# Optimization experiments

Hardware: AMD Instinct MI355X
Metric: run time of the kernel (lower is better)

The kernel has to match this reference:

```python
import jax, jax.numpy as jnp
import numpy as np

DIM = 64
HEADS = 8
K_RATIOS = [0.5, 0.67, 0.75, 0.8]
BN_EPS = 1e-5


def conv3d(x, w, b, groups=1, pad=0):
    out = jax.lax.conv_general_dilated(
        x, w, window_strides=(1, 1, 1), padding=[(pad, pad)] * 3,
        dimension_numbers=('NCDHW', 'OIDHW', 'NCDHW'),
        feature_group_count=groups)
    return out + b[None, :, None, None, None]


def bn_eval(x, gamma, beta):
    # BatchNorm3d in inference mode with init running stats (mean=0, var=1)
    s = gamma / np.float32(np.sqrt(1.0 + BN_EPS))
    return x * s[None, :, None, None, None] + beta[None, :, None, None, None]


def setup_inputs() -> dict:
    key = jax.random.key(0)
    ks = jax.random.split(key, 12)
    def p(k, shape, scale=0.05):
        return jax.random.normal(k, shape, dtype=jnp.float32) * scale
    B, D, H, W = 2, 16, 64, 64
    return {
        'x': jax.random.normal(ks[0], (B, DIM, D, H, W), dtype=jnp.float32),
        'w_qkv': p(ks[1], (3 * DIM, DIM, 1, 1, 1)),
        'b_qkv': p(ks[2], (3 * DIM,)),
        'w_dw': p(ks[3], (3 * DIM, 1, 3, 3, 3)),
        'b_dw': p(ks[4], (3 * DIM,)),
        'temperature': jnp.ones((HEADS, 1, 1), jnp.float32),
        'attn_weights': jnp.ones((len(K_RATIOS),), jnp.float32),
        'w_recal': p(ks[5], (DIM, DIM, 1, 1, 1)),
        'b_recal': p(ks[6], (DIM,)),
        'bn1_g': jnp.ones((DIM,), jnp.float32),
        'bn1_b': jnp.zeros((DIM,), jnp.float32),
        'w_fus': p(ks[7], (DIM, 2 * DIM, 1, 1, 1)),
        'b_fus': p(ks[8], (DIM,)),
        'bn2_g': jnp.ones((DIM,), jnp.float32),
        'bn2_b': jnp.zeros((DIM,), jnp.float32),
        'w_proj': p(ks[9], (DIM, DIM, 1, 1, 1)),
        'b_proj': p(ks[10], (DIM,)),
    }


def reference(x, w_qkv, b_qkv, w_dw, b_dw, temperature, attn_weights,
              w_recal, b_recal, bn1_g, bn1_b, w_fus, b_fus, bn2_g, bn2_b,
              w_proj, b_proj):
    b, c, d, h, w = x.shape
    residual = x
    qkv = conv3d(conv3d(x, w_qkv, b_qkv), w_dw, b_dw, groups=3 * DIM, pad=1)
    q, k, v = jnp.split(qkv, 3, axis=1)
    def to_heads(t):  # b (head ch) d h w -> b head ch (d h w)
        return t.reshape(b, HEADS, c // HEADS, d * h * w)
    q, k, v = to_heads(q), to_heads(k), to_heads(v)
    # L2-normalize along token dim (torch F.normalize, eps=1e-12)
    q = q / jnp.maximum(jnp.linalg.norm(q, axis=-1, keepdims=True), 1e-12)
    k = k / jnp.maximum(jnp.linalg.norm(k, axis=-1, keepdims=True), 1e-12)
    C = q.shape[2]
    attn = jnp.einsum('bhin,bhjn->bhij', q, k) * temperature[None]  # (b,head,C,C)
    soft_w = jax.nn.softmax(attn_weights)
    weighted = 0.0
    for i, ratio in enumerate(K_RATIOS):
        kv = int(C * ratio)
        idx = jax.lax.top_k(attn, kv)[1]                      # (b,head,C,kv)
        mask = jax.nn.one_hot(idx, C, dtype=attn.dtype).sum(-2) > 0
        probs = jax.nn.softmax(jnp.where(mask, attn, -jnp.inf), axis=-1)
        out = jnp.einsum('bhij,bhjn->bhin', probs, v)          # (b,head,C,N)
        weighted = weighted + soft_w[i] * out.reshape(b, c, d, h, w)
    recalib = jax.nn.sigmoid(bn_eval(conv3d(weighted, w_recal, b_recal), bn1_g, bn1_b))
    enhanced = weighted * recalib
    fused = jnp.concatenate([enhanced, residual], axis=1)
    output = bn_eval(conv3d(fused, w_fus, b_fus), bn2_g, bn2_b)
    output = conv3d(output, w_proj, b_proj)
    return output
```

## Files before the change

### kernel.cpp

```cpp
#include <hip/hip_runtime.h>
#include <math.h>

#define NPOS 65536
#define DD 16
#define HHH 64
#define WWW 64
#define K3CHUNK 64

typedef __attribute__((ext_vector_type(8))) short bf16x8;
typedef __attribute__((ext_vector_type(4))) short s16x4;
typedef __attribute__((ext_vector_type(4))) float f32x4;
typedef __attribute__((ext_vector_type(2))) _Float16 f16x2;

static __device__ __forceinline__ short f2bf(float f) {
    union { float f; unsigned u; } v; v.f = f;
    unsigned r = (v.u + 0x7FFFu + ((v.u >> 16) & 1u)) >> 16;
    return (short)r;
}
static __device__ __forceinline__ float bf2f(short s) {
    union { unsigned u; float f; } v; v.u = ((unsigned)(unsigned short)s) << 16;
    return v.f;
}
static __device__ __forceinline__ f16x2 i2h(int i) {
    union { int i; f16x2 h; } v; v.i = i; return v.h;
}
static __device__ __forceinline__ int h2i(f16x2 h) {
    union { int i; f16x2 h; } v; v.h = h; return v.i;
}
static __device__ __forceinline__ float fdot2f(f16x2 a, f16x2 b, float c) {
#if __has_builtin(__builtin_amdgcn_fdot2)
    return __builtin_amdgcn_fdot2(a, b, c, false);
#else
    return fmaf((float)a[0], (float)b[0], fmaf((float)a[1], (float)b[1], c));
#endif
}

__global__ void k0_prep(const float* __restrict__ Wq,
                        const float* __restrict__ Wr, const float* __restrict__ Wf,
                        const float* __restrict__ Wp,
                        const float* __restrict__ brec,
                        const float* __restrict__ bn1g, const float* __restrict__ bn1b,
                        const float* __restrict__ bfus,
                        const float* __restrict__ bn2g, const float* __restrict__ bn2b,
                        short* __restrict__ WqA, short* __restrict__ WrA,
                        short* __restrict__ WfA, short* __restrict__ WpA,
                        float* __restrict__ bias1, float* __restrict__ bias2) {
    const float invs = 1.0f / sqrtf(1.0f + 1e-5f);
    int idx = blockIdx.x * 256 + threadIdx.x;
    if (idx < 12288) {
        int e = idx & 7, l = (idx >> 3) & 63, m = (idx >> 9) & 3;
        int t = (idx >> 11) & 1, c = idx >> 12;
        int out = c*64 + 16*m + (l & 15), k = 32*t + ((l >> 4) << 3) + e;
        WqA[idx] = f2bf(Wq[out*64 + k]);
        return;
    }
    int i = idx - 12288;
    if (i < 4096) {
        int e = i & 7, l = (i >> 3) & 63, m = (i >> 9) & 3, t = (i >> 11) & 1;
        int out = 16*m + (l & 15), k = 32*t + ((l >> 4) << 3) + e;
        WrA[i] = f2bf(Wr[out*64 + k] * bn1g[out] * invs);
        return;
    }
    i -= 4096;
    if (i < 8192) {
        int e = i & 7, l = (i >> 3) & 63, m = (i >> 9) & 3, t = (i >> 11) & 3;
        int out = 16*m + (l & 15), k = 32*t + ((l >> 4) << 3) + e;
        WfA[i] = f2bf(Wf[out*128 + k] * bn2g[out] * invs);
        return;
    }
    i -= 8192;
    if (i < 4096) {
        int e = i & 7, l = (i >> 3) & 63, m = (i >> 9) & 3, t = (i >> 11) & 1;
        int out = 16*m + (l & 15), k = 32*t + ((l >> 4) << 3) + e;
        WpA[i] = f2bf(Wp[out*64 + k]);
        return;
    }
    i -= 4096;
    if (i < 64)       bias1[i]    = brec[i]    * bn1g[i]    * invs + bn1b[i];
    else if (i < 128) bias2[i-64] = bfus[i-64] * bn2g[i-64] * invs + bn2b[i-64];
}

__global__ __launch_bounds__(256) void k1_qkv(const float* __restrict__ x,
        const short* __restrict__ WqA, const float* __restrict__ bq,
        short* __restrict__ qkv) {
    __shared__ __align__(16) float Xs[64 * 64];
    const int tid = threadIdx.x, lane = tid & 63, wv = tid >> 6;
    const int blk = blockIdx.x;
    const int b = blk >> 10, n0 = (blk & 1023) << 6;
    const float* xg = x + ((long long)b * 64) * NPOS + n0;
    #pragma unroll
    for (int kk = 0; kk < 4; ++kk) {
        int idx = tid + kk * 256;
        int ch = idx >> 4, p = (idx & 15) << 2;
        *(float4*)(Xs + ch * 64 + p) = *(const float4*)(xg + (long long)ch * NPOS + p);
    }
    const int bcol  = wv * 16 + (lane & 15);
    const int bk    = (lane >> 4) << 3;
    const int drow0 = (lane >> 4) << 2;
    __syncthreads();

    bf16x8 B0, B1;
    #pragma unroll
    for (int e = 0; e < 8; ++e) B0[e] = f2bf(Xs[(bk + e) * 64 + bcol]);
    #pragma unroll
    for (int e = 0; e < 8; ++e) B1[e] = f2bf(Xs[(32 + bk + e) * 64 + bcol]);

    short* outb = qkv + ((long long)b * 192) * NPOS + n0 + bcol;
    #pragma unroll
    for (int c = 0; c < 3; ++c) {
        #pragma unroll
        for (int m = 0; m < 4; ++m) {
            bf16x8 A0 = *(const bf16x8*)(WqA + (((c * 2 + 0) * 4 + m) * 64 + lane) * 8);
            bf16x8 A1 = *(const bf16x8*)(WqA + (((c * 2 + 1) * 4 + m) * 64 + lane) * 8);
            f32x4 a = {0.f, 0.f, 0.f, 0.f};
            a = __builtin_amdgcn_mfma_f32_16x16x32_bf16(A0, B0, a, 0, 0, 0);
            a = __builtin_amdgcn_mfma_f32_16x16x32_bf16(A1, B1, a, 0, 0, 0);
            float4 bb = *(const float4*)(bq + c * 64 + 16 * m + drow0);
            a[0] += bb.x; a[1] += bb.y; a[2] += bb.z; a[3] += bb.w;
            #pragma unroll
            for (int r = 0; r < 4; ++r)
                outb[(long long)(c * 64 + 16 * m + drow0 + r) * NPOS] = f2bf(a[r]);
        }
    }
}

__global__ __launch_bounds__(256) void k2_dw(const short* __restrict__ qkv,
        const float* __restrict__ Wd, const float* __restrict__ bd,
        short* __restrict__ qkv2) {
    __shared__ __align__(16) _Float16 tile[108 * 72];
    __shared__ unsigned wpk01[9], wpk2z[9];
    __shared__ float bsh[1];
    const int tid = threadIdx.x;
    const int lane = tid & 63;
    const int bc  = blockIdx.x >> 4;
    const int sub = blockIdx.x & 15;
    const int d0  = (sub >> 2) << 2;
    const int h0  = (sub & 3) << 4;
    const int c   = bc % 192;

    if (tid < 9) {
        const float* wb = Wd + c * 27 + tid * 3;
        f16x2 a = {(_Float16)wb[0], (_Float16)wb[1]};
        f16x2 z = {(_Float16)wb[2], (_Float16)0.f};
        wpk01[tid] = (unsigned)h2i(a);
        wpk2z[tid] = (unsigned)h2i(z);
    }
    if (tid == 31) bsh[0] = bd[c];

    const short* in = qkv + (long long)bc * NPOS;
    for (int i = tid; i < 864; i += 256) {
        const int r = i >> 3, q8 = i & 7;
        const int dd = r / 18;
        const int hh = r - dd * 18;
        const int d = d0 + dd - 1;
        const int h = h0 + hh - 1;
        union { f16x2 h[4]; int4 i4; } u;
        u.i4 = make_int4(0, 0, 0, 0);
        if (d >= 0 && d < DD && h >= 0 && h < HHH) {
            bf16x8 raw = *(const bf16x8*)(in + (d << 12) + (h << 6) + (q8 << 3));
            #pragma unroll
            for (int e = 0; e < 4; ++e) {
                f16x2 hp = {(_Float16)bf2f(raw[2 * e]), (_Float16)bf2f(raw[2 * e + 1])};
                u.h[e] = hp;
            }
        }
        *(int4*)(tile + r * 72 + (q8 << 3)) = u.i4;
    }
    __syncthreads();

    unsigned w01r[9], w2zr[9];
    #pragma unroll
    for (int s = 0; s < 9; ++s) { w01r[s] = wpk01[s]; w2zr[s] = wpk2z[s]; }
    const float bias = bsh[0];

    const int wl = tid & 15;
    const int oh = tid >> 4;
    const int w0 = wl << 2;

    float acc[4][4];
    #pragma unroll
    for (int od = 0; od < 4; ++od)
        #pragma unroll
        for (int j = 0; j < 4; ++j) acc[od][j] = bias;

    #pragma unroll
    for (int kh = 0; kh < 3; ++kh) {
        #pragma unroll
        for (int dp = 0; dp < 6; ++dp) {
            const int2 dd2 = *(const int2*)(tile + (dp * 18 + oh + kh) * 72 + w0);
            int Ldw = __shfl(dd2.y, (lane + 63) & 63, 64);
            int Rdw = __shfl(dd2.x, (lane + 1) & 63, 64);
            Ldw = (wl == 0)  ? 0 : Ldw;
            Rdw = (wl == 15) ? 0 : Rdw;
            int pr[5];
            pr[0] = __builtin_amdgcn_alignbit(dd2.x, Ldw, 16);
            pr[1] = dd2.x;
            pr[2] = __builtin_amdgcn_alignbit(dd2.y, dd2.x, 16);
            pr[3] = dd2.y;
            pr[4] = __builtin_amdgcn_alignbit(Rdw, dd2.y, 16);
            #pragma unroll
            for (int od = 0; od < 4; ++od) {
                const int kd = dp - od;
                if (kd < 0 || kd > 2) continue;
                const f16x2 w01 = i2h((int)w01r[kd * 3 + kh]);
                const f16x2 w2z = i2h((int)w2zr[kd * 3 + kh]);
                #pragma unroll
                for (int j = 0; j < 4; ++j) {
                    acc[od][j] = fdot2f(w01, i2h(pr[j]), acc[od][j]);
                    acc[od][j] = fdot2f(w2z, i2h(pr[j + 2]), acc[od][j]);
                }
            }
        }
    }
    short* outp = qkv2 + (long long)bc * NPOS + (h0 + oh) * 64 + w0;
    #pragma unroll
    for (int od = 0; od < 4; ++od) {
        s16x4 o;
        #pragma unroll
        for (int j = 0; j < 4; ++j) o[j] = f2bf(acc[od][j]);
        *(s16x4*)(outp + ((d0 + od) << 12)) = o;
    }
}

__global__ __launch_bounds__(256) void k3_gram(const short* __restrict__ qkv2,
                                               float* __restrict__ partial) {
    const int blk = blockIdx.x;
    const int chunk = blk & (K3CHUNK - 1);
    const int bh = blk >> 6;
    const int b = bh >> 3, h = bh & 7;
    const int tid = threadIdx.x, lane = tid & 63, wv = tid >> 6;
    const short* base = qkv2 + ((long long)b * 192 + h * 8) * NPOS;
    const int ch = lane & 15;
    const long long roff = (ch < 8 ? (long long)ch : (long long)(56 + ch)) * NPOS;
    const short* p = base + roff + chunk * 1024 + wv * 256 + ((lane >> 4) << 3);

    f32x4 a0 = {0.f, 0.f, 0.f, 0.f}, a1 = {0.f, 0.f, 0.f, 0.f};
    #pragma unroll
    for (int it = 0; it < 4; ++it) {
        bf16x8 f0 = *(const bf16x8*)(p + it * 64);
        bf16x8 f1 = *(const bf16x8*)(p + it * 64 + 32);
        a0 = __builtin_amdgcn_mfma_f32_16x16x32_bf16(f0, f0, a0, 0, 0, 0);
        a1 = __builtin_amdgcn_mfma_f32_16x16x32_bf16(f1, f1, a1, 0, 0, 0);
    }
    __shared__ float gs[4][256];
    #pragma unroll
    for (int r = 0; r < 4; ++r)
        gs[wv][(((lane >> 4) << 2) + r) * 16 + (lane & 15)] = a0[r] + a1[r];
    __syncthreads();
    const int row = tid >> 4, col = tid & 15;
    float v = gs[0][tid] + gs[1][tid] + gs[2][tid] + gs[3][tid];
    float* pp = partial + ((long long)bh * K3CHUNK + chunk) * 80;
    if (row < 8 && col >= 8)      pp[row * 8 + (col - 8)] = v;
    else if (row == col && row < 8) pp[64 + row] = v;
    else if (row == col)            pp[72 + row - 8] = v;
}

__global__ void k3b_reduce(const float* __restrict__ partial, float* __restrict__ gram) {
    int s = blockIdx.x * 256 + threadIdx.x;
    if (s >= 16 * 80) return;
    int bh = s / 80, slot = s % 80;
    float acc = 0.f;
    for (int c = 0; c < K3CHUNK; ++c)
        acc += partial[((long long)bh * K3CHUNK + c) * 80 + slot];
    gram[s] = acc;
}

__global__ void k4_combine(const float* __restrict__ gram, const float* __restrict__ temp,
                           const float* __restrict__ aw, float* __restrict__ P) {
    int t = threadIdx.x;
    if (t >= 128) return;
    int bh = t >> 3, i = t & 7;
    int h = bh & 7;
    const float* g = gram + bh * 80;
    float qn = fmaxf(sqrtf(g[64 + i]), 1e-12f);
    float tp = temp[h];
    float attn[8];
    #pragma unroll
    for (int j = 0; j < 8; ++j) {
        float kn = fmaxf(sqrtf(g[72 + j]), 1e-12f);
        attn[j] = g[i * 8 + j] / (qn * kn) * tp;
    }
    float awv[4];
    float am = -3.4e38f;
    for (int r = 0; r < 4; ++r) { awv[r] = aw[r]; am = fmaxf(am, awv[r]); }
    float asum = 0.f;
    for (int r = 0; r < 4; ++r) { awv[r] = expf(awv[r] - am); asum += awv[r]; }
    const int kvs[4] = {4, 5, 6, 6};
    float Pacc[8];
    #pragma unroll
    for (int j = 0; j < 8; ++j) Pacc[j] = 0.f;
    for (int r = 0; r < 4; ++r) {
        float sw = awv[r] / asum;
        int kv = kvs[r];
        bool sel[8];
        #pragma unroll
        for (int j = 0; j < 8; ++j) sel[j] = false;
        for (int m = 0; m < kv; ++m) {
            int best = 0; float bv = -3.4e38f;
            for (int j = 0; j < 8; ++j)
                if (!sel[j] && attn[j] > bv) { bv = attn[j]; best = j; }
            sel[best] = true;
        }
        float mx = -3.4e38f;
        for (int j = 0; j < 8; ++j) if (sel[j]) mx = fmaxf(mx, attn[j]);
        float es = 0.f, e[8];
        for (int j = 0; j < 8; ++j) { e[j] = sel[j] ? expf(attn[j] - mx) : 0.f; es += e[j]; }
        for (int j = 0; j < 8; ++j) Pacc[j] += sw * e[j] / es;
    }
    for (int j = 0; j < 8; ++j) P[t * 8 + j] = Pacc[j];
}

__global__ void k4b_pfrag(const float* __restrict__ P, short* __restrict__ PA) {
    int idx = blockIdx.x * 256 + threadIdx.x;
    int e = idx & 7, l = (idx >> 3) & 63, m = (idx >> 9) & 3;
    int t = (idx >> 11) & 1, b = idx >> 12;
    int out = 16*m + (l & 15), k = 32*t + ((l >> 4) << 3) + e;
    float v = ((k >> 3) == (out >> 3)) ? P[(b * 64 + out) * 8 + (k & 7)] : 0.f;
    PA[idx] = f2bf(v);
}

__global__ __launch_bounds__(256) void k5_tail(
        const short* __restrict__ qkv2, const float* __restrict__ x,
        const short* __restrict__ PA, const short* __restrict__ WrA,
        const short* __restrict__ WfA, const short* __restrict__ WpA,
        const float* __restrict__ bias1, const float* __restrict__ bias2,
        const float* __restrict__ bp, float* __restrict__ out) {
    __shared__ __align__(16) float As[64 * 64];
    __shared__ __align__(16) float Xs[64 * 64];
    const int tid = threadIdx.x, lane = tid & 63, wv = tid >> 6;
    const int blk = blockIdx.x;
    const int b = blk >> 10, n0 = (blk & 1023) << 6;
    const short* vg = qkv2 + ((long long)b * 192 + 128) * NPOS + n0;
    const float* xg = x + ((long long)b * 64) * NPOS + n0;
    #pragma unroll
    for (int kk = 0; kk < 4; ++kk) {
        int idx = tid + kk * 256;
        int ch = idx >> 4, p = (idx & 15) << 2;
        *(float4*)(Xs + ch * 64 + p) = *(const float4*)(xg + (long long)ch * NPOS + p);
    }
    #pragma unroll
    for (int kk = 0; kk < 2; ++kk) {
        int i = tid + kk * 256;
        int ch = i >> 3, p0 = (i & 7) << 3;
        bf16x8 raw = *(const bf16x8*)(vg + (long long)ch * NPOS + p0);
        *(float4*)(As + ch * 64 + p0) =
            make_float4(bf2f(raw[0]), bf2f(raw[1]), bf2f(raw[2]), bf2f(raw[3]));
        *(float4*)(As + ch * 64 + p0 + 4) =
            make_float4(bf2f(raw[4]), bf2f(raw[5]), bf2f(raw[6]), bf2f(raw[7]));
    }
    bf16x8 pA[2][4];
    #pragma unroll
    for (int t = 0; t < 2; ++t)
        #pragma unroll
        for (int m = 0; m < 4; ++m)
            pA[t][m] = *(const bf16x8*)(PA + (((b * 2 + t) * 4 + m) * 64 + lane) * 8);
    const int bcol  = wv * 16 + (lane & 15);
    const int bk    = (lane >> 4) << 3;
    const int drow0 = (lane >> 4) << 2;
    __syncthreads();

    auto loadB = [&](const float* S, int kbase) {
        bf16x8 r;
        #pragma unroll
        for (int e = 0; e < 8; ++e) r[e] = f2bf(S[(kbase + bk + e) * 64 + bcol]);
        return r;
    };

    f32x4 Dw[4];
    {
        bf16x8 B0 = loadB(As, 0), B1 = loadB(As, 32);
        #pragma unroll
        for (int m = 0; m < 4; ++m) {
            f32x4 a = {0.f, 0.f, 0.f, 0.f};
            a = __builtin_amdgcn_mfma_f32_16x16x32_bf16(pA[0][m], B0, a, 0, 0, 0);
            a = __builtin_amdgcn_mfma_f32_16x16x32_bf16(pA[1][m], B1, a, 0, 0, 0);
            Dw[m] = a;
        }
    }
    #pragma unroll
    for (int m = 0; m < 4; ++m)
        #pragma unroll
        for (int r = 0; r < 4; ++r)
            As[(16 * m + drow0 + r) * 64 + bcol] = Dw[m][r];

    float enh[4][4];
    {
        bf16x8 rA[2][4];
        #pragma unroll
        for (int t = 0; t < 2; ++t)
            #pragma unroll
            for (int m = 0; m < 4; ++m)
                rA[t][m] = *(const bf16x8*)(WrA + ((t * 4 + m) * 64 + lane) * 8);
        bf16x8 B0 = loadB(As, 0), B1 = loadB(As, 32);
        #pragma unroll
        for (int m = 0; m < 4; ++m) {
            f32x4 a = {0.f, 0.f, 0.f, 0.f};
            a = __builtin_amdgcn_mfma_f32_16x16x32_bf16(rA[0][m], B0, a, 0, 0, 0);
            a = __builtin_amdgcn_mfma_f32_16x16x32_bf16(rA[1][m], B1, a, 0, 0, 0);
            #pragma unroll
            for (int r = 0; r < 4; ++r) {
                float z = a[r] + bias1[16 * m + drow0 + r];
                enh[m][r] = Dw[m][r] / (1.f + expf(-z));
            }
        }
    }
    #pragma unroll
    for (int m = 0; m < 4; ++m)
        #pragma unroll
        for (int r = 0; r < 4; ++r)
            As[(16 * m + drow0 + r) * 64 + bcol] = enh[m][r];

    f32x4 D3[4];
    {
        bf16x8 fA[4][4];
        #pragma unroll
        for (int t = 0; t < 4; ++t)
            #pragma unroll
            for (int m = 0; m < 4; ++m)
                fA[t][m] = *(const bf16x8*)(WfA + ((t * 4 + m) * 64 + lane) * 8);
        bf16x8 B0 = loadB(As, 0), B1 = loadB(As, 32);
        bf16x8 B2 = loadB(Xs, 0), B3 = loadB(Xs, 32);
        #pragma unroll
        for (int m = 0; m < 4; ++m) {
            f32x4 a = {0.f, 0.f, 0.f, 0.f};
            a = __builtin_amdgcn_mfma_f32_16x16x32_bf16(fA[0][m], B0, a, 0, 0, 0);
            a = __builtin_amdgcn_mfma_f32_16x16x32_bf16(fA[1][m], B1, a, 0, 0, 0);
            a = __builtin_amdgcn_mfma_f32_16x16x32_bf16(fA[2][m], B2, a, 0, 0, 0);
            a = __builtin_amdgcn_mfma_f32_16x16x32_bf16(fA[3][m], B3, a, 0, 0, 0);
            #pragma unroll
            for (int r = 0; r < 4; ++r) a[r] += bias2[16 * m + drow0 + r];
            D3[m] = a;
        }
    }
    #pragma unroll
    for (int m = 0; m < 4; ++m)
        #pragma unroll
        for (int r = 0; r < 4; ++r)
            As[(16 * m + drow0 + r) * 64 + bcol] = D3[m][r];

    {
        bf16x8 qA[2][4];
        #pragma unroll
        for (int t = 0; t < 2; ++t)
            #pragma unroll
            for (int m = 0; m < 4; ++m)
                qA[t][m] = *(const bf16x8*)(WpA + ((t * 4 + m) * 64 + lane) * 8);
        bf16x8 B0 = loadB(As, 0), B1 = loadB(As, 32);
        float* outb = out + ((long long)b * 64) * NPOS + n0 + bcol;
        #pragma unroll
        for (int m = 0; m < 4; ++m) {
            f32x4 a = {0.f, 0.f, 0.f, 0.f};
            a = __builtin_amdgcn_mfma_f32_16x16x32_bf16(qA[0][m], B0, a, 0, 0, 0);
            a = __builtin_amdgcn_mfma_f32_16x16x32_bf16(qA[1][m], B1, a, 0, 0, 0);
            #pragma unroll
            for (int r = 0; r < 4; ++r)
                outb[(long long)(16 * m + drow0 + r) * NPOS] =
                    a[r] + bp[16 * m + drow0 + r];
        }
    }
}

extern "C" void kernel_launch(void* const* d_in, const int* in_sizes, int n_in,
                              void* d_out, int out_size, void* d_ws, size_t ws_size,
                              hipStream_t stream) {
    (void)in_sizes; (void)n_in; (void)out_size; (void)ws_size;
    const float* x     = (const float*)d_in[0];
    const float* w_qkv = (const float*)d_in[1];
    const float* b_qkv = (const float*)d_in[2];
    const float* w_dw  = (const float*)d_in[3];
    const float* b_dw  = (const float*)d_in[4];
    const float* temp  = (const float*)d_in[5];
    const float* aw    = (const float*)d_in[6];
    const float* w_rec = (const float*)d_in[7];
    const float* b_rec = (const float*)d_in[8];
    const float* bn1g  = (const float*)d_in[9];
    const float* bn1b  = (const float*)d_in[10];
    const float* w_fus = (const float*)d_in[11];
    const float* b_fus = (const float*)d_in[12];
    const float* bn2g  = (const float*)d_in[13];
    const float* bn2b  = (const float*)d_in[14];
    const float* w_prj = (const float*)d_in[15];
    const float* b_prj = (const float*)d_in[16];
    float* out = (float*)d_out;

    short* qkv  = (short*)d_ws;
    short* qkv2 = qkv + 25165824;
    float* part = (float*)(qkv2 + 25165824);
    float* gram = part + 163840;
    float* P    = gram + 1280;
    float* bias1 = P + 1024;
    float* bias2 = bias1 + 64;
    short* WqA  = (short*)(bias2 + 64);
    short* WrA  = WqA + 12288;
    short* WfA  = WrA + 4096;
    short* WpA  = WfA + 8192;
    short* PAb  = WpA + 4096;

    k0_prep<<<113, 256, 0, stream>>>(w_qkv, w_rec, w_fus, w_prj, b_rec, bn1g, bn1b,
                                     b_fus, bn2g, bn2b, WqA, WrA, WfA, WpA, bias1, bias2);
    k1_qkv<<<2048, 256, 0, stream>>>(x, WqA, b_qkv, qkv);
    k2_dw<<<6144, 256, 0, stream>>>(qkv, w_dw, b_dw, qkv2);
    k3_gram<<<16 * K3CHUNK, 256, 0, stream>>>(qkv2, part);
    k3b_reduce<<<5, 256, 0, stream>>>(part, gram);
    k4_combine<<<1, 128, 0, stream>>>(gram, temp, aw, P);
    k4b_pfrag<<<32, 256, 0, stream>>>(P, PAb);
    k5_tail<<<2048, 256, 0, stream>>>(qkv2, x, PAb, WrA, WfA, WpA,
                                      bias1, bias2, b_prj, out);
}
```

Measured before the change: 109.9 us.

## Switch intermediates to fp16 MFMA and fuse gram reduce, combine, pfrag kernels

Moves every intermediate buffer and MFMA from bf16 to fp16. This lets the depthwise conv tile load copy raw fp16 data straight into shared memory, where it previously converted bf16 to fp16 element by element. It also merges the three small kernels (gram reduction, top-k softmax combine, P fragment packing) into a single one-block kernel, removing two launches and their global round trips. The cost is fp16's narrower range on the activations, and the fused reduction now runs on only one block instead of five.

```diff
diff --git a/kernel.cpp b/kernel.cpp
--- a/kernel.cpp
+++ b/kernel.cpp
@@ -7,19 +7,16 @@
 #define WWW 64
 #define K3CHUNK 64
 
-typedef __attribute__((ext_vector_type(8))) short bf16x8;
+typedef __attribute__((ext_vector_type(8))) _Float16 h16x8;
 typedef __attribute__((ext_vector_type(4))) short s16x4;
 typedef __attribute__((ext_vector_type(4))) float f32x4;
 typedef __attribute__((ext_vector_type(2))) _Float16 f16x2;
 
-static __device__ __forceinline__ short f2bf(float f) {
-    union { float f; unsigned u; } v; v.f = f;
-    unsigned r = (v.u + 0x7FFFu + ((v.u >> 16) & 1u)) >> 16;
-    return (short)r;
-}
-static __device__ __forceinline__ float bf2f(short s) {
-    union { unsigned u; float f; } v; v.u = ((unsigned)(unsigned short)s) << 16;
-    return v.f;
+static __device__ __forceinline__ short f2h(float f) {
+    union { _Float16 h; short s; } v; v.h = (_Float16)f; return v.s;
+}
+static __device__ __forceinline__ float h2f(short s) {
+    union { short s; _Float16 h; } v; v.s = s; return (float)v.h;
 }
 static __device__ __forceinline__ f16x2 i2h(int i) {
     union { int i; f16x2 h; } v; v.i = i; return v.h;
@@ -51,28 +48,28 @@
         int e = idx & 7, l = (idx >> 3) & 63, m = (idx >> 9) & 3;
         int t = (idx >> 11) & 1, c = idx >> 12;
         int out = c*64 + 16*m + (l & 15), k = 32*t + ((l >> 4) << 3) + e;
-        WqA[idx] = f2bf(Wq[out*64 + k]);
+        WqA[idx] = f2h(Wq[out*64 + k]);
         return;
     }
     int i = idx - 12288;
     if (i < 4096) {
         int e = i & 7, l = (i >> 3) & 63, m = (i >> 9) & 3, t = (i >> 11) & 1;
         int out = 16*m + (l & 15), k = 32*t + ((l >> 4) << 3) + e;
-        WrA[i] = f2bf(Wr[out*64 + k] * bn1g[out] * invs);
+        WrA[i] = f2h(Wr[out*64 + k] * bn1g[out] * invs);
         return;
     }
     i -= 4096;
     if (i < 8192) {
         int e = i & 7, l = (i >> 3) & 63, m = (i >> 9) & 3, t = (i >> 11) & 3;
         int out = 16*m + (l & 15), k = 32*t + ((l >> 4) << 3) + e;
-        WfA[i] = f2bf(Wf[out*128 + k] * bn2g[out] * invs);
+        WfA[i] = f2h(Wf[out*128 + k] * bn2g[out] * invs);
         return;
     }
     i -= 8192;
     if (i < 4096) {
         int e = i & 7, l = (i >> 3) & 63, m = (i >> 9) & 3, t = (i >> 11) & 1;
         int out = 16*m + (l & 15), k = 32*t + ((l >> 4) << 3) + e;
-        WpA[i] = f2bf(Wp[out*64 + k]);
+        WpA[i] = f2h(Wp[out*64 + k]);
         return;
     }
     i -= 4096;
@@ -99,27 +96,27 @@
     const int drow0 = (lane >> 4) << 2;
     __syncthreads();
 
-    bf16x8 B0, B1;
-    #pragma unroll
-    for (int e = 0; e < 8; ++e) B0[e] = f2bf(Xs[(bk + e) * 64 + bcol]);
-    #pragma unroll
-    for (int e = 0; e < 8; ++e) B1[e] = f2bf(Xs[(32 + bk + e) * 64 + bcol]);
+    h16x8 B0, B1;
+    #pragma unroll
+    for (int e = 0; e < 8; ++e) B0[e] = (_Float16)Xs[(bk + e) * 64 + bcol];
+    #pragma unroll
+    for (int e = 0; e < 8; ++e) B1[e] = (_Float16)Xs[(32 + bk + e) * 64 + bcol];
 
     short* outb = qkv + ((long long)b * 192) * NPOS + n0 + bcol;
     #pragma unroll
     for (int c = 0; c < 3; ++c) {
         #pragma unroll
         for (int m = 0; m < 4; ++m) {
-            bf16x8 A0 = *(const bf16x8*)(WqA + (((c * 2 + 0) * 4 + m) * 64 + lane) * 8);
-            bf16x8 A1 = *(const bf16x8*)(WqA + (((c * 2 + 1) * 4 + m) * 64 + lane) * 8);
+            h16x8 A0 = *(const h16x8*)(WqA + (((c * 2 + 0) * 4 + m) * 64 + lane) * 8);
+            h16x8 A1 = *(const h16x8*)(WqA + (((c * 2 + 1) * 4 + m) * 64 + lane) * 8);
             f32x4 a = {0.f, 0.f, 0.f, 0.f};
-            a = __builtin_amdgcn_mfma_f32_16x16x32_bf16(A0, B0, a, 0, 0, 0);
-            a = __builtin_amdgcn_mfma_f32_16x16x32_bf16(A1, B1, a, 0, 0, 0);
+            a = __builtin_amdgcn_mfma_f32_16x16x32_f16(A0, B0, a, 0, 0, 0);
+            a = __builtin_amdgcn_mfma_f32_16x16x32_f16(A1, B1, a, 0, 0, 0);
             float4 bb = *(const float4*)(bq + c * 64 + 16 * m + drow0);
             a[0] += bb.x; a[1] += bb.y; a[2] += bb.z; a[3] += bb.w;
             #pragma unroll
             for (int r = 0; r < 4; ++r)
-                outb[(long long)(c * 64 + 16 * m + drow0 + r) * NPOS] = f2bf(a[r]);
+                outb[(long long)(c * 64 + 16 * m + drow0 + r) * NPOS] = f2h(a[r]);
         }
     }
 }
@@ -154,17 +151,10 @@
         const int hh = r - dd * 18;
         const int d = d0 + dd - 1;
         const int h = h0 + hh - 1;
-        union { f16x2 h[4]; int4 i4; } u;
-        u.i4 = make_int4(0, 0, 0, 0);
-        if (d >= 0 && d < DD && h >= 0 && h < HHH) {
-            bf16x8 raw = *(const bf16x8*)(in + (d << 12) + (h << 6) + (q8 << 3));
-            #pragma unroll
-            for (int e = 0; e < 4; ++e) {
-                f16x2 hp = {(_Float16)bf2f(raw[2 * e]), (_Float16)bf2f(raw[2 * e + 1])};
-                u.h[e] = hp;
-            }
-        }
-        *(int4*)(tile + r * 72 + (q8 << 3)) = u.i4;
+        int4 u = make_int4(0, 0, 0, 0);
+        if (d >= 0 && d < DD && h >= 0 && h < HHH)
+            u = *(const int4*)(in + (d << 12) + (h << 6) + (q8 << 3));
+        *(int4*)(tile + r * 72 + (q8 << 3)) = u;
     }
     __syncthreads();
 
@@ -217,7 +207,7 @@
     for (int od = 0; od < 4; ++od) {
         s16x4 o;
         #pragma unroll
-        for (int j = 0; j < 4; ++j) o[j] = f2bf(acc[od][j]);
+        for (int j = 0; j < 4; ++j) o[j] = f2h(acc[od][j]);
         *(s16x4*)(outp + ((d0 + od) << 12)) = o;
     }
 }
@@ -237,10 +227,10 @@
     f32x4 a0 = {0.f, 0.f, 0.f, 0.f}, a1 = {0.f, 0.f, 0.f, 0.f};
     #pragma unroll
     for (int it = 0; it < 4; ++it) {
-        bf16x8 f0 = *(const bf16x8*)(p + it * 64);
-        bf16x8 f1 = *(const bf16x8*)(p + it * 64 + 32);
-        a0 = __builtin_amdgcn_mfma_f32_16x16x32_bf16(f0, f0, a0, 0, 0, 0);
-        a1 = __builtin_amdgcn_mfma_f32_16x16x32_bf16(f1, f1, a1, 0, 0, 0);
+        h16x8 f0 = *(const h16x8*)(p + it * 64);
+        h16x8 f1 = *(const h16x8*)(p + it * 64 + 32);
+        a0 = __builtin_amdgcn_mfma_f32_16x16x32_f16(f0, f0, a0, 0, 0, 0);
+        a1 = __builtin_amdgcn_mfma_f32_16x16x32_f16(f1, f1, a1, 0, 0, 0);
     }
     __shared__ float gs[4][256];
     #pragma unroll
@@ -255,68 +245,69 @@
     else if (row == col)            pp[72 + row - 8] = v;
 }
 
-__global__ void k3b_reduce(const float* __restrict__ partial, float* __restrict__ gram) {
-    int s = blockIdx.x * 256 + threadIdx.x;
-    if (s >= 16 * 80) return;
-    int bh = s / 80, slot = s % 80;
-    float acc = 0.f;
-    for (int c = 0; c < K3CHUNK; ++c)
-        acc += partial[((long long)bh * K3CHUNK + c) * 80 + slot];
-    gram[s] = acc;
-}
-
-__global__ void k4_combine(const float* __restrict__ gram, const float* __restrict__ temp,
-                           const float* __restrict__ aw, float* __restrict__ P) {
-    int t = threadIdx.x;
-    if (t >= 128) return;
-    int bh = t >> 3, i = t & 7;
-    int h = bh & 7;
-    const float* g = gram + bh * 80;
-    float qn = fmaxf(sqrtf(g[64 + i]), 1e-12f);
-    float tp = temp[h];
-    float attn[8];
-    #pragma unroll
-    for (int j = 0; j < 8; ++j) {
-        float kn = fmaxf(sqrtf(g[72 + j]), 1e-12f);
-        attn[j] = g[i * 8 + j] / (qn * kn) * tp;
-    }
-    float awv[4];
-    float am = -3.4e38f;
-    for (int r = 0; r < 4; ++r) { awv[r] = aw[r]; am = fmaxf(am, awv[r]); }
-    float asum = 0.f;
-    for (int r = 0; r < 4; ++r) { awv[r] = expf(awv[r] - am); asum += awv[r]; }
-    const int kvs[4] = {4, 5, 6, 6};
-    float Pacc[8];
-    #pragma unroll
-    for (int j = 0; j < 8; ++j) Pacc[j] = 0.f;
-    for (int r = 0; r < 4; ++r) {
-        float sw = awv[r] / asum;
-        int kv = kvs[r];
-        bool sel[8];
-        #pragma unroll
-        for (int j = 0; j < 8; ++j) sel[j] = false;
-        for (int m = 0; m < kv; ++m) {
-            int best = 0; float bv = -3.4e38f;
-            for (int j = 0; j < 8; ++j)
-                if (!sel[j] && attn[j] > bv) { bv = attn[j]; best = j; }
-            sel[best] = true;
-        }
-        float mx = -3.4e38f;
-        for (int j = 0; j < 8; ++j) if (sel[j]) mx = fmaxf(mx, attn[j]);
-        float es = 0.f, e[8];
-        for (int j = 0; j < 8; ++j) { e[j] = sel[j] ? expf(attn[j] - mx) : 0.f; es += e[j]; }
-        for (int j = 0; j < 8; ++j) Pacc[j] += sw * e[j] / es;
-    }
-    for (int j = 0; j < 8; ++j) P[t * 8 + j] = Pacc[j];
-}
-
-__global__ void k4b_pfrag(const float* __restrict__ P, short* __restrict__ PA) {
-    int idx = blockIdx.x * 256 + threadIdx.x;
-    int e = idx & 7, l = (idx >> 3) & 63, m = (idx >> 9) & 3;
-    int t = (idx >> 11) & 1, b = idx >> 12;
-    int out = 16*m + (l & 15), k = 32*t + ((l >> 4) << 3) + e;
-    float v = ((k >> 3) == (out >> 3)) ? P[(b * 64 + out) * 8 + (k & 7)] : 0.f;
-    PA[idx] = f2bf(v);
+__global__ __launch_bounds__(256) void k34_combine(const float* __restrict__ partial,
+        const float* __restrict__ temp, const float* __restrict__ aw,
+        short* __restrict__ PA) {
+    __shared__ float gram[1280];
+    __shared__ float P[1024];
+    const int tid = threadIdx.x;
+    for (int s = tid; s < 1280; s += 256) {
+        int bh = s / 80, slot = s % 80;
+        float acc = 0.f;
+        for (int c = 0; c < K3CHUNK; ++c)
+            acc += partial[((long long)bh * K3CHUNK + c) * 80 + slot];
+        gram[s] = acc;
+    }
+    __syncthreads();
+    if (tid < 128) {
+        int bh = tid >> 3, i = tid & 7;
+        int h = bh & 7;
+        const float* g = gram + bh * 80;
+        float qn = fmaxf(sqrtf(g[64 + i]), 1e-12f);
+        float tp = temp[h];
+        float attn[8];
+        #pragma unroll
+        for (int j = 0; j < 8; ++j) {
+            float kn = fmaxf(sqrtf(g[72 + j]), 1e-12f);
+            attn[j] = g[i * 8 + j] / (qn * kn) * tp;
+        }
+        float awv[4];
+        float am = -3.4e38f;
+        for (int r = 0; r < 4; ++r) { awv[r] = aw[r]; am = fmaxf(am, awv[r]); }
+        float asum = 0.f;
+        for (int r = 0; r < 4; ++r) { awv[r] = expf(awv[r] - am); asum += awv[r]; }
+        const int kvs[4] = {4, 5, 6, 6};
+        float Pacc[8];
+        #pragma unroll
+        for (int j = 0; j < 8; ++j) Pacc[j] = 0.f;
+        for (int r = 0; r < 4; ++r) {
+            float sw = awv[r] / asum;
+            int kv = kvs[r];
+            bool sel[8];
+            #pragma unroll
+            for (int j = 0; j < 8; ++j) sel[j] = false;
+            for (int m = 0; m < kv; ++m) {
+                int best = 0; float bv = -3.4e38f;
+                for (int j = 0; j < 8; ++j)
+                    if (!sel[j] && attn[j] > bv) { bv = attn[j]; best = j; }
+                sel[best] = true;
+            }
+            float mx = -3.4e38f;
+            for (int j = 0; j < 8; ++j) if (sel[j]) mx = fmaxf(mx, attn[j]);
+            float es = 0.f, e[8];
+            for (int j = 0; j < 8; ++j) { e[j] = sel[j] ? expf(attn[j] - mx) : 0.f; es += e[j]; }
+            for (int j = 0; j < 8; ++j) Pacc[j] += sw * e[j] / es;
+        }
+        for (int j = 0; j < 8; ++j) P[tid * 8 + j] = Pacc[j];
+    }
+    __syncthreads();
+    for (int idx = tid; idx < 8192; idx += 256) {
+        int e = idx & 7, l = (idx >> 3) & 63, m = (idx >> 9) & 3;
+        int t = (idx >> 11) & 1, b = idx >> 12;
+        int out = 16*m + (l & 15), k = 32*t + ((l >> 4) << 3) + e;
+        float v = ((k >> 3) == (out >> 3)) ? P[(b * 64 + out) * 8 + (k & 7)] : 0.f;
+        PA[idx] = f2h(v);
+    }
 }
 
 __global__ __launch_bounds__(256) void k5_tail(
@@ -342,38 +333,38 @@
     for (int kk = 0; kk < 2; ++kk) {
         int i = tid + kk * 256;
         int ch = i >> 3, p0 = (i & 7) << 3;
-        bf16x8 raw = *(const bf16x8*)(vg + (long long)ch * NPOS + p0);
+        h16x8 raw = *(const h16x8*)(vg + (long long)ch * NPOS + p0);
         *(float4*)(As + ch * 64 + p0) =
-            make_float4(bf2f(raw[0]), bf2f(raw[1]), bf2f(raw[2]), bf2f(raw[3]));
+            make_float4((float)raw[0], (float)raw[1], (float)raw[2], (float)raw[3]);
         *(float4*)(As + ch * 64 + p0 + 4) =
-            make_float4(bf2f(raw[4]), bf2f(raw[5]), bf2f(raw[6]), bf2f(raw[7]));
-    }
-    bf16x8 pA[2][4];
+            make_float4((float)raw[4], (float)raw[5], (float)raw[6], (float)raw[7]);
+    }
+    h16x8 pA[2][4];
     #pragma unroll
     for (int t = 0; t < 2; ++t)
         #pragma unroll
         for (int m = 0; m < 4; ++m)
-            pA[t][m] = *(const bf16x8*)(PA + (((b * 2 + t) * 4 + m) * 64 + lane) * 8);
+            pA[t][m] = *(const h16x8*)(PA + (((b * 2 + t) * 4 + m) * 64 + lane) * 8);
     const int bcol  = wv * 16 + (lane & 15);
     const int bk    = (lane >> 4) << 3;
     const int drow0 = (lane >> 4) << 2;
     __syncthreads();
 
     auto loadB = [&](const float* S, int kbase) {
-        bf16x8 r;
-        #pragma unroll
-        for (int e = 0; e < 8; ++e) r[e] = f2bf(S[(kbase + bk + e) * 64 + bcol]);
+        h16x8 r;
+        #pragma unroll
+        for (int e = 0; e < 8; ++e) r[e] = (_Float16)S[(kbase + bk + e) * 64 + bcol];
         return r;
     };
 
     f32x4 Dw[4];
     {
-        bf16x8 B0 = loadB(As, 0), B1 = loadB(As, 32);
+        h16x8 B0 = loadB(As, 0), B1 = loadB(As, 32);
         #pragma unroll
         for (int m = 0; m < 4; ++m) {
             f32x4 a = {0.f, 0.f, 0.f, 0.f};
-            a = __builtin_amdgcn_mfma_f32_16x16x32_bf16(pA[0][m], B0, a, 0, 0, 0);
-            a = __builtin_amdgcn_mfma_f32_16x16x32_bf16(pA[1][m], B1, a, 0, 0, 0);
+            a = __builtin_amdgcn_mfma_f32_16x16x32_f16(pA[0][m], B0, a, 0, 0, 0);
+            a = __builtin_amdgcn_mfma_f32_16x16x32_f16(pA[1][m], B1, a, 0, 0, 0);
             Dw[m] = a;
         }
     }
@@ -385,18 +376,18 @@
 
     float enh[4][4];
     {
-        bf16x8 rA[2][4];
+        h16x8 rA[2][4];
         #pragma unroll
         for (int t = 0; t < 2; ++t)
             #pragma unroll
             for (int m = 0; m < 4; ++m)
-                rA[t][m] = *(const bf16x8*)(WrA + ((t * 4 + m) * 64 + lane) * 8);
-        bf16x8 B0 = loadB(As, 0), B1 = loadB(As, 32);
+                rA[t][m] = *(const h16x8*)(WrA + ((t * 4 + m) * 64 + lane) * 8);
+        h16x8 B0 = loadB(As, 0), B1 = loadB(As, 32);
         #pragma unroll
         for (int m = 0; m < 4; ++m) {
             f32x4 a = {0.f, 0.f, 0.f, 0.f};
-            a = __builtin_amdgcn_mfma_f32_16x16x32_bf16(rA[0][m], B0, a, 0, 0, 0);
-            a = __builtin_amdgcn_mfma_f32_16x16x32_bf16(rA[1][m], B1, a, 0, 0, 0);
+            a = __builtin_amdgcn_mfma_f32_16x16x32_f16(rA[0][m], B0, a, 0, 0, 0);
+            a = __builtin_amdgcn_mfma_f32_16x16x32_f16(rA[1][m], B1, a, 0, 0, 0);
             #pragma unroll
             for (int r = 0; r < 4; ++r) {
                 float z = a[r] + bias1[16 * m + drow0 + r];
@@ -412,21 +403,21 @@
 
     f32x4 D3[4];
     {
-        bf16x8 fA[4][4];
+        h16x8 fA[4][4];
         #pragma unroll
         for (int t = 0; t < 4; ++t)
             #pragma unroll
             for (int m = 0; m < 4; ++m)
-                fA[t][m] = *(const bf16x8*)(WfA + ((t * 4 + m) * 64 + lane) * 8);
-        bf16x8 B0 = loadB(As, 0), B1 = loadB(As, 32);
-        bf16x8 B2 = loadB(Xs, 0), B3 = loadB(Xs, 32);
+                fA[t][m] = *(const h16x8*)(WfA + ((t * 4 + m) * 64 + lane) * 8);
+        h16x8 B0 = loadB(As, 0), B1 = loadB(As, 32);
+        h16x8 B2 = loadB(Xs, 0), B3 = loadB(Xs, 32);
         #pragma unroll
         for (int m = 0; m < 4; ++m) {
             f32x4 a = {0.f, 0.f, 0.f, 0.f};
-            a = __builtin_amdgcn_mfma_f32_16x16x32_bf16(fA[0][m], B0, a, 0, 0, 0);
-            a = __builtin_amdgcn_mfma_f32_16x16x32_bf16(fA[1][m], B1, a, 0, 0, 0);
-            a = __builtin_amdgcn_mfma_f32_16x16x32_bf16(fA[2][m], B2, a, 0, 0, 0);
-            a = __builtin_amdgcn_mfma_f32_16x16x32_bf16(fA[3][m], B3, a, 0, 0, 0);
+            a = __builtin_amdgcn_mfma_f32_16x16x32_f16(fA[0][m], B0, a, 0, 0, 0);
+            a = __builtin_amdgcn_mfma_f32_16x16x32_f16(fA[1][m], B1, a, 0, 0, 0);
+            a = __builtin_amdgcn_mfma_f32_16x16x32_f16(fA[2][m], B2, a, 0, 0, 0);
+            a = __builtin_amdgcn_mfma_f32_16x16x32_f16(fA[3][m], B3, a, 0, 0, 0);
             #pragma unroll
             for (int r = 0; r < 4; ++r) a[r] += bias2[16 * m + drow0 + r];
             D3[m] = a;
@@ -439,19 +430,19 @@
             As[(16 * m + drow0 + r) * 64 + bcol] = D3[m][r];
 
     {
-        bf16x8 qA[2][4];
+        h16x8 qA[2][4];
         #pragma unroll
         for (int t = 0; t < 2; ++t)
             #pragma unroll
             for (int m = 0; m < 4; ++m)
-                qA[t][m] = *(const bf16x8*)(WpA + ((t * 4 + m) * 64 + lane) * 8);
-        bf16x8 B0 = loadB(As, 0), B1 = loadB(As, 32);
+                qA[t][m] = *(const h16x8*)(WpA + ((t * 4 + m) * 64 + lane) * 8);
+        h16x8 B0 = loadB(As, 0), B1 = loadB(As, 32);
         float* outb = out + ((long long)b * 64) * NPOS + n0 + bcol;
         #pragma unroll
         for (int m = 0; m < 4; ++m) {
             f32x4 a = {0.f, 0.f, 0.f, 0.f};
-            a = __builtin_amdgcn_mfma_f32_16x16x32_bf16(qA[0][m], B0, a, 0, 0, 0);
-            a = __builtin_amdgcn_mfma_f32_16x16x32_bf16(qA[1][m], B1, a, 0, 0, 0);
+            a = __builtin_amdgcn_mfma_f32_16x16x32_f16(qA[0][m], B0, a, 0, 0, 0);
+            a = __builtin_amdgcn_mfma_f32_16x16x32_f16(qA[1][m], B1, a, 0, 0, 0);
             #pragma unroll
             for (int r = 0; r < 4; ++r)
                 outb[(long long)(16 * m + drow0 + r) * NPOS] =
@@ -486,9 +477,7 @@
     short* qkv  = (short*)d_ws;
     short* qkv2 = qkv + 25165824;
     float* part = (float*)(qkv2 + 25165824);
-    float* gram = part + 163840;
-    float* P    = gram + 1280;
-    float* bias1 = P + 1024;
+    float* bias1 = part + 81920;
     float* bias2 = bias1 + 64;
     short* WqA  = (short*)(bias2 + 64);
     short* WrA  = WqA + 12288;
@@ -501,9 +490,7 @@
     k1_qkv<<<2048, 256, 0, stream>>>(x, WqA, b_qkv, qkv);
     k2_dw<<<6144, 256, 0, stream>>>(qkv, w_dw, b_dw, qkv2);
     k3_gram<<<16 * K3CHUNK, 256, 0, stream>>>(qkv2, part);
-    k3b_reduce<<<5, 256, 0, stream>>>(part, gram);
-    k4_combine<<<1, 128, 0, stream>>>(gram, temp, aw, P);
-    k4b_pfrag<<<32, 256, 0, stream>>>(P, PAb);
+    k34_combine<<<1, 256, 0, stream>>>(part, temp, aw, PAb);
     k5_tail<<<2048, 256, 0, stream>>>(qkv2, x, PAb, WrA, WfA, WpA,
                                       bias1, bias2, b_prj, out);
 }
```

After: 110.4 us. No clear change (+0.5%).
